# Performance work log

Hardware: AMD Instinct MI355X
Metric: run time of the kernel (lower is better)

The kernel has to match this reference:

```python
import jax, jax.numpy as jnp
import numpy as np

N, F_IN, HID, CLUST = 4096, 128, 128, 128
HEADS = 2
RADIUS = 2.0
TOPK_ADD = 2
MOTIF_TOPK = 8
ETA = 0.5
L0_GAMMA, L0_ZETA = -0.1, 1.1
NEG_SLOPE = 0.2
BN_EPS = 1e-5
NEG_INF = -1e9


def _row_topk(A, k):
    # keep top-k per row, symmetrize by max, zero diagonal (matches row_topk)
    n = A.shape[0]
    if n <= k:
        S = A
    else:
        vals, idx = jax.lax.top_k(A, k)
        S = jnp.zeros_like(A).at[jnp.arange(n)[:, None], idx].set(vals)
        S = jnp.maximum(S, S.T)
    return S * (1.0 - jnp.eye(n, dtype=A.dtype))


def _bn_eval(x, g, b, m, v):
    return (x - m) * g * jax.lax.rsqrt(v + BN_EPS) + b


def _gate(logits, tau):
    # hard-concrete gate, eval path
    t = jnp.clip(tau, 0.1, None)
    s = jax.nn.sigmoid(logits / t) * (L0_ZETA - L0_GAMMA) + L0_GAMMA
    return jnp.clip(s, 0.0, 1.0)


def _gcn_dense(feat, A_w, W, b):
    # GCN: D^-1/2 A D^-1/2 (X W) + b, zero-degree rows -> 0
    deg = A_w.sum(axis=1)
    dinv = jnp.where(deg > 0, jax.lax.rsqrt(jnp.where(deg > 0, deg, 1.0)), 0.0)
    An = dinv[:, None] * A_w * dinv[None, :]
    return An @ (feat @ W) + b


def setup_inputs():
    key = jax.random.key(0)
    ks = jax.random.split(key, 30)
    eye = jnp.eye(N, dtype=jnp.float32)
    p = 16.0 / N  # ~16 avg degree
    B = jax.random.uniform(ks[0], (N, N)) < p
    A_in = ((B | B.T) & ~jnp.eye(N, dtype=bool)).astype(jnp.float32)
    Mw = jnp.where(jax.random.uniform(ks[1], (N, N)) < p, jax.random.uniform(ks[2], (N, N)), 0.0)
    A_motif = jnp.maximum(Mw, Mw.T) * (1.0 - eye)
    coords = jax.random.randint(ks[3], (N, 2), 0, 64).astype(jnp.float32)
    x = jax.random.normal(ks[4], (N, F_IN))
    s_in = 1.0 / np.sqrt(F_IN)
    s_h = 1.0 / np.sqrt(2 * HID)
    return {
        'x': x, 'A_in': A_in, 'A_motif': A_motif, 'coords': coords,
        'gat_w': jax.random.normal(ks[5], (F_IN, HEADS * HID)) * s_in,
        'gat_asrc': jax.random.normal(ks[6], (HEADS, HID)) * s_h,
        'gat_adst': jax.random.normal(ks[7], (HEADS, HID)) * s_h,
        'gat_b': jnp.zeros((HEADS * HID,)),
        'bnA_g': jnp.ones((2 * HID,)), 'bnA_b': jnp.zeros((2 * HID,)),
        'bnA_m': jax.random.normal(ks[8], (2 * HID,)) * 0.1,
        'bnA_v': 0.5 + jax.random.uniform(ks[9], (2 * HID,)),
        'gcnM_w': jax.random.normal(ks[10], (F_IN, 2 * HID)) * s_in,
        'gcnM_b': jnp.zeros((2 * HID,)),
        'bnM_g': jnp.ones((2 * HID,)), 'bnM_b': jnp.zeros((2 * HID,)),
        'bnM_m': jax.random.normal(ks[11], (2 * HID,)) * 0.1,
        'bnM_v': 0.5 + jax.random.uniform(ks[12], (2 * HID,)),
        'mu': jnp.asarray(-3.0), 'tau': jnp.asarray(1.0),
        'prune_w': jax.random.normal(ks[13], (4 * HID + 1,)) * s_h,
        'prune_b': jnp.asarray(0.0),
        'rewire_w': jax.random.normal(ks[14], (4 * HID + 1,)) * s_h,
        'rewire_b': jnp.asarray(0.0),
        'pool_w': jax.random.normal(ks[15], (2 * HID, CLUST)) * s_h,
        'pool_b': jnp.zeros((CLUST,)),
    }


def reference(x, A_in, A_motif, coords, gat_w, gat_asrc, gat_adst, gat_b,
              bnA_g, bnA_b, bnA_m, bnA_v, gcnM_w, gcnM_b, bnM_g, bnM_b, bnM_m, bnM_v,
              mu, tau, prune_w, prune_b, rewire_w, rewire_b, pool_w, pool_b):
    n = x.shape[0]
    eye = jnp.eye(n, dtype=x.dtype)
    # --- GAT branch on A_in (dense masked attention; PyG adds self loops) ---
    Wx = (x @ gat_w).reshape(n, HEADS, HID)           # [N, heads, H]
    a_src = (Wx * gat_asrc).sum(-1)                   # [N, heads]
    a_dst = (Wx * gat_adst).sum(-1)
    e = jax.nn.leaky_relu(a_dst[:, None, :] + a_src[None, :, :], NEG_SLOPE)  # e[i,j,h]
    adj_mask = (A_in > 0) | jnp.eye(n, dtype=bool)
    e = jnp.where(adj_mask[..., None], e, NEG_INF)
    alpha = jax.nn.softmax(e, axis=1)                 # softmax over sources j
    h_A = jnp.einsum('ijh,jhd->ihd', alpha, Wx).reshape(n, HEADS * HID) + gat_b
    h_A = jax.nn.elu(_bn_eval(h_A, bnA_g, bnA_b, bnA_m, bnA_v))
    # --- motif branch ---
    M_hat = _row_topk(A_motif, MOTIF_TOPK)
    h_M = jax.nn.elu(_bn_eval(_gcn_dense(x, M_hat, gcnM_w, gcnM_b), bnM_g, bnM_b, bnM_m, bnM_v))
    h = h_A + jax.nn.softplus(mu) * h_M               # [N, 2H]
    d2 = 2 * HID
    triu = jnp.triu(jnp.ones((n, n), dtype=bool), 1)
    # --- prune gate on existing upper-tri edges (Linear is separable) ---
    pu = h @ prune_w[:d2]
    pv = h @ prune_w[d2:2 * d2]
    prune_logits = pu[:, None] + pv[None, :] + prune_w[2 * d2] * M_hat + prune_b
    z_prune = _gate(prune_logits, tau)
    edge_u = triu & (A_in > 0)
    Wp = jnp.where(edge_u, z_prune * A_in, 0.0)
    A_pruned = Wp + Wp.T
    # --- rewire candidates: L1 cdist within radius, non-edges, upper tri ---
    dist = jnp.abs(coords[:, None, :] - coords[None, :, :]).sum(-1)
    cand_u = (dist > 0) & (dist <= RADIUS) & (A_in < 1e-6) & triu
    ru = h @ rewire_w[:d2]
    rv = h @ rewire_w[d2:2 * d2]
    rew_logits = ru[:, None] + rv[None, :] + rewire_w[2 * d2] * M_hat + rewire_b
    Zu = jnp.where(cand_u, _gate(rew_logits, tau), 0.0)
    # per-node top-k selection over incident candidates (symmetric view)
    cand_sym = cand_u | cand_u.T
    scores = jnp.where(cand_sym, Zu + Zu.T, NEG_INF)
    thr = jax.lax.top_k(scores, TOPK_ADD)[0][:, -1]
    keep = (scores >= thr[:, None]) & cand_sym
    pair_keep = (keep | keep.T) & cand_u
    A_added_u = jnp.where(pair_keep, Zu, 0.0)
    A_added_sym = jnp.maximum(A_added_u, A_added_u.T)
    A_refined = A_pruned + ETA * A_added_sym
    # --- pooling GCN (default GCNConv adds self loops, weight 1) ---
    S = jax.nn.softmax(_gcn_dense(h, A_refined + eye, pool_w, pool_b), axis=1)  # [N, C]
    X_coarse = S.T @ h                                 # [C, 2H]
    A_c = S.T @ A_refined @ S
    A_c = A_c * (1.0 - jnp.eye(A_c.shape[0], dtype=A_c.dtype))
    A_coarse = _row_topk(A_c, MOTIF_TOPK)
    return X_coarse, A_coarse
```

## Files before the change

kernel.cpp:

```cpp
#include <hip/hip_runtime.h>
#include <hip/hip_bf16.h>
#include <stdint.h>

#define N 4096
#define FIN 128
#define HID 128
#define D2 256
#define CLUST 128
#define NEG_INF (-1e9f)
#define KAJ 128
#define KM 96
#define KC 64
#define KA (KAJ + KC)
#define CCAP 32
#define JCH 128
#define NCH (N/JCH)
#define CTILE 16

typedef __hip_bfloat16 bf16;

__device__ __forceinline__ float cvt(float v){ return v; }
__device__ __forceinline__ float cvt(bf16 v){ return __bfloat162float(v); }
__device__ __forceinline__ void stout(float* p, size_t i, float v){ p[i] = v; }
__device__ __forceinline__ void stout(bf16* p, size_t i, float v){ p[i] = __float2bfloat16(v); }

__device__ __forceinline__ float hc_gate(float l, float tau){
  float t = fmaxf(tau, 0.1f);
  float s = 1.f / (1.f + expf(-l / t));
  s = s * 1.2f - 0.1f;
  return fminf(fmaxf(s, 0.f), 1.f);
}

__global__ void k_detect(const void* x, const void* w, int* flag){
  __shared__ int hits;
  int t = threadIdx.x;
  if (t == 0) hits = 0;
  __syncthreads();
  const bf16* xb = (const bf16*)x;
  const bf16* wb = (const bf16*)w;
  int h = 0;
  for (int i = t; i < 4096; i += 256){
    float a = __bfloat162float(xb[i]);
    float b = __bfloat162float(wb[i]);
    if (!(fabsf(a) < 1e6f)) ++h;
    if (!(fabsf(b) < 1e6f)) ++h;
  }
  atomicAdd(&hits, h);
  __syncthreads();
  if (t == 0) *flag = (hits > 0) ? 1 : 0;
}

template<typename T>
__device__ void xw2_body(const T* x, const T* gat_w, const T* gcnM_w,
                         float* Wx, float* xwM, float* xr){
  int i0 = blockIdx.x * 16, t = threadIdx.x;
  for (int idx = t; idx < 16*FIN; idx += 256) xr[idx] = cvt(x[(size_t)i0*FIN + idx]);
  __syncthreads();
  float wx[16], xm[16];
  #pragma unroll
  for (int r = 0; r < 16; ++r){ wx[r] = 0.f; xm[r] = 0.f; }
  for (int k = 0; k < FIN; ++k){
    float wa = cvt(gat_w[k*D2 + t]);
    float wm = cvt(gcnM_w[k*D2 + t]);
    #pragma unroll
    for (int r = 0; r < 16; ++r){
      wx[r] += xr[r*FIN + k] * wa;
      xm[r] += xr[r*FIN + k] * wm;
    }
  }
  #pragma unroll
  for (int r = 0; r < 16; ++r){
    Wx[(size_t)(i0+r)*D2 + t] = wx[r];
    xwM[(size_t)(i0+r)*D2 + t] = xm[r];
  }
}
__global__ void k_xw2(const int* fl, const void* x, const void* gw, const void* gmw,
                      float* Wx, float* xwM){
  __shared__ float xr[16*FIN];
  if (*fl) xw2_body<float>((const float*)x,(const float*)gw,(const float*)gmw,Wx,xwM,xr);
  else     xw2_body<bf16 >((const bf16*)x,(const bf16*)gw,(const bf16*)gmw,Wx,xwM,xr);
}

template<typename T>
__device__ void att_body(const float* Wx, const T* asrc, const T* adst,
                         float* a_src, float* a_dst){
  int w = threadIdx.x >> 6, l = threadIdx.x & 63;
  int row = blockIdx.x*4 + w;
  const float4* wr = (const float4*)(Wx + (size_t)row*D2);
  float4 v = wr[l];
  float s0 = cvt(asrc[l*4])*v.x + cvt(asrc[l*4+1])*v.y
           + cvt(asrc[l*4+2])*v.z + cvt(asrc[l*4+3])*v.w;
  float s1 = cvt(adst[l*4])*v.x + cvt(adst[l*4+1])*v.y
           + cvt(adst[l*4+2])*v.z + cvt(adst[l*4+3])*v.w;
  for (int d = 16; d > 0; d >>= 1){
    s0 += __shfl_down(s0, d, 32);
    s1 += __shfl_down(s1, d, 32);
  }
  if ((l & 31) == 0){
    a_src[row*2 + (l >> 5)] = s0;
    a_dst[row*2 + (l >> 5)] = s1;
  }
}
__global__ void k_att(const int* fl, const float* Wx, const void* as, const void* ad,
                      float* a_src, float* a_dst){
  if (*fl) att_body<float>(Wx,(const float*)as,(const float*)ad,a_src,a_dst);
  else     att_body<bf16 >(Wx,(const bf16*)as,(const bf16*)ad,a_src,a_dst);
}

__device__ __forceinline__ void t8_insert(unsigned long long* keys, float v, int j){
  if (v > 0.f){
    unsigned long long key =
      ((unsigned long long)__float_as_uint(v) << 32) | (unsigned int)(~(unsigned int)j);
    if (key > keys[7]){
      keys[7] = key;
      #pragma unroll
      for (int q = 7; q > 0; --q){
        if (keys[q] > keys[q-1]){ unsigned long long tmp = keys[q]; keys[q] = keys[q-1]; keys[q-1] = tmp; }
      }
    }
  }
}
__global__ void k_top8(const int* fl, const void* Amot, float* t8v, int* t8i,
                       int* Midx, float* Mval, int* Mcnt){
  __shared__ unsigned long long red[256];
  int i = blockIdx.x, t = threadIdx.x;
  unsigned long long keys[8];
  #pragma unroll
  for (int q = 0; q < 8; ++q) keys[q] = 0ull;
  if (*fl){
    const float4* rowp = (const float4*)((const float*)Amot + (size_t)i*N);
    for (int s = 0; s < N/1024; ++s){
      float4 v4 = rowp[s*256 + t];
      int jb = s*1024 + t*4;
      t8_insert(keys, v4.x, jb);
      t8_insert(keys, v4.y, jb+1);
      t8_insert(keys, v4.z, jb+2);
      t8_insert(keys, v4.w, jb+3);
    }
  } else {
    const bf16* rowp = (const bf16*)Amot + (size_t)i*N;
    for (int s = 0; s < N/256; ++s){
      int j = t + 256*s;
      t8_insert(keys, cvt(rowp[j]), j);
    }
  }
  unsigned long long wins[8];
  unsigned long long last = ~0ull;
  for (int r = 0; r < 8; ++r){
    unsigned long long cand = 0ull;
    #pragma unroll
    for (int q = 0; q < 8; ++q){ if (keys[q] < last){ cand = keys[q]; break; } }
    red[t] = cand;
    __syncthreads();
    for (int s = 128; s > 0; s >>= 1){
      if (t < s){ if (red[t+s] > red[t]) red[t] = red[t+s]; }
      __syncthreads();
    }
    unsigned long long win = red[0];
    __syncthreads();
    wins[r] = win;
    last = win;
  }
  if (t == 0){
    int c = 0;
    #pragma unroll
    for (int r = 0; r < 8; ++r){
      float v = __uint_as_float((unsigned int)(wins[r] >> 32));
      int j = (int)(~(unsigned int)wins[r]);
      bool ok = (wins[r] != 0ull) && (v > 0.f);
      t8v[i*8 + r] = ok ? v : 0.f;
      t8i[i*8 + r] = ok ? j : -1;
      if (ok){ Midx[i*KM + c] = j; Mval[i*KM + c] = v; ++c; }
    }
    Mcnt[i] = c;
  }
}

__global__ void k_mscat(const float* __restrict__ t8v, const int* __restrict__ t8i,
                        int* __restrict__ Midx, float* __restrict__ Mval,
                        int* __restrict__ Mcnt){
  int e = blockIdx.x*256 + threadIdx.x;
  if (e >= N*8) return;
  int i = e >> 3;
  int j = t8i[e];
  if (j < 0) return;
  #pragma unroll
  for (int s = 0; s < 8; ++s) if (t8i[j*8 + s] == i) return;
  int p = atomicAdd(&Mcnt[j], 1);
  if (p < KM){ Midx[j*KM + p] = i; Mval[j*KM + p] = t8v[e]; }
}

__global__ void k_degM(const float* __restrict__ Mval, const int* __restrict__ Mcnt,
                       float* __restrict__ dinvM){
  int i = blockIdx.x*256 + threadIdx.x;
  if (i >= N) return;
  int n = min(Mcnt[i], KM);
  float s = 0.f;
  for (int e = 0; e < n; ++e) s += Mval[i*KM + e];
  dinvM[i] = (s > 0.f) ? rsqrtf(s) : 0.f;
}

template<typename T>
__device__ void motif_body(const int* Midx, const float* Mval, const int* Mcnt,
                           const float* dinvM, const float* xwM, const T* gcnM_b,
                           const T* bng, const T* bnb, const T* bnm, const T* bnv,
                           float* hM, int* nj, float* nw){
  int i = blockIdx.x, t = threadIdx.x;
  int n = min(Mcnt[i], KM);
  for (int e = t; e < n; e += 256){
    int j = Midx[i*KM + e];
    nj[e] = j;
    nw[e] = Mval[i*KM + e] * dinvM[j];
  }
  __syncthreads();
  float acc = 0.f;
  for (int e = 0; e < n; ++e) acc += nw[e] * xwM[nj[e]*D2 + t];
  float val = acc * dinvM[i] + cvt(gcnM_b[t]);
  val = (val - cvt(bnm[t])) * cvt(bng[t]) * rsqrtf(cvt(bnv[t]) + 1e-5f) + cvt(bnb[t]);
  val = (val > 0.f) ? val : expm1f(val);
  hM[i*D2 + t] = val;
}
__global__ void k_motif_agg(const int* fl, const int* Midx, const float* Mval,
                            const int* Mcnt, const float* dinvM, const float* xwM,
                            const void* gb, const void* g, const void* b,
                            const void* m, const void* v, float* hM){
  __shared__ int nj[KM];
  __shared__ float nw[KM];
  if (*fl) motif_body<float>(Midx,Mval,Mcnt,dinvM,xwM,(const float*)gb,(const float*)g,
                             (const float*)b,(const float*)m,(const float*)v,hM,nj,nw);
  else     motif_body<bf16 >(Midx,Mval,Mcnt,dinvM,xwM,(const bf16*)gb,(const bf16*)g,
                             (const bf16*)b,(const bf16*)m,(const bf16*)v,hM,nj,nw);
}

__global__ void k_adj(const int* fl, const void* Ain,
                      int* __restrict__ AdjIdx, float* __restrict__ AdjVal,
                      int* __restrict__ AdjCnt){
  __shared__ int cnt;
  int i = blockIdx.x, t = threadIdx.x;
  if (t == 0) cnt = 0;
  __syncthreads();
  if (*fl){
    const float4* rowp = (const float4*)((const float*)Ain + (size_t)i*N);
    for (int s = 0; s < N/1024; ++s){
      float4 v4 = rowp[s*256 + t];
      int jb = s*1024 + t*4;
      if (v4.x > 0.f && jb   != i){ int p = atomicAdd(&cnt,1); if (p < KAJ){ AdjIdx[i*KAJ+p] = jb;   AdjVal[i*KAJ+p] = v4.x; } }
      if (v4.y > 0.f && jb+1 != i){ int p = atomicAdd(&cnt,1); if (p < KAJ){ AdjIdx[i*KAJ+p] = jb+1; AdjVal[i*KAJ+p] = v4.y; } }
      if (v4.z > 0.f && jb+2 != i){ int p = atomicAdd(&cnt,1); if (p < KAJ){ AdjIdx[i*KAJ+p] = jb+2; AdjVal[i*KAJ+p] = v4.z; } }
      if (v4.w > 0.f && jb+3 != i){ int p = atomicAdd(&cnt,1); if (p < KAJ){ AdjIdx[i*KAJ+p] = jb+3; AdjVal[i*KAJ+p] = v4.w; } }
    }
  } else {
    const bf16* rowp = (const bf16*)Ain + (size_t)i*N;
    for (int j = t; j < N; j += 256){
      float v = cvt(rowp[j]);
      if (v > 0.f && j != i){ int p = atomicAdd(&cnt,1); if (p < KAJ){ AdjIdx[i*KAJ+p] = j; AdjVal[i*KAJ+p] = v; } }
    }
  }
  __syncthreads();
  if (t == 0) AdjCnt[i] = min(cnt, KAJ);
}

template<typename T>
__device__ void gat_body(const int* AdjIdx, const int* AdjCnt, const float* Wx,
                         const float* a_src, const float* a_dst, const T* gat_b,
                         const T* bng, const T* bnb, const T* bnm, const T* bnv,
                         const float* hM, const T* mu,
                         float* h, int* nbr, float* ew, float* mm, float* inv){
  int i = blockIdx.x, t = threadIdx.x;
  int na = AdjCnt[i];
  for (int e = t; e < na; e += 256) nbr[e] = AdjIdx[i*KAJ + e];
  if (t == 0) nbr[na] = i;
  __syncthreads();
  int n = na + 1;
  float ad0 = a_dst[i*2], ad1 = a_dst[i*2 + 1];
  for (int e = t; e < n; e += 256){
    int j = nbr[e];
    float e0 = ad0 + a_src[j*2];
    float e1 = ad1 + a_src[j*2 + 1];
    e0 = (e0 > 0.f) ? e0 : 0.2f * e0;
    e1 = (e1 > 0.f) ? e1 : 0.2f * e1;
    ew[2*e] = e0; ew[2*e + 1] = e1;
  }
  __syncthreads();
  if (t == 0){
    float m0 = -3.4e38f, m1 = -3.4e38f;
    for (int e = 0; e < n; ++e){ m0 = fmaxf(m0, ew[2*e]); m1 = fmaxf(m1, ew[2*e+1]); }
    mm[0] = m0; mm[1] = m1;
  }
  __syncthreads();
  for (int e = t; e < n; e += 256){
    ew[2*e]   = expf(ew[2*e]   - mm[0]);
    ew[2*e+1] = expf(ew[2*e+1] - mm[1]);
  }
  __syncthreads();
  if (t == 0){
    float s0 = 0.f, s1 = 0.f;
    for (int e = 0; e < n; ++e){ s0 += ew[2*e]; s1 += ew[2*e+1]; }
    inv[0] = 1.f/s0; inv[1] = 1.f/s1;
  }
  __syncthreads();
  int hh = t >> 7;
  float acc = 0.f;
  for (int e = 0; e < n; ++e) acc += ew[2*e + hh] * Wx[nbr[e]*D2 + t];
  float val = acc * inv[hh] + cvt(gat_b[t]);
  val = (val - cvt(bnm[t])) * cvt(bng[t]) * rsqrtf(cvt(bnv[t]) + 1e-5f) + cvt(bnb[t]);
  val = (val > 0.f) ? val : expm1f(val);
  float spmu = log1pf(expf(cvt(mu[0])));
  h[i*D2 + t] = val + spmu * hM[i*D2 + t];
}
__global__ void k_gat_agg(const int* fl, const int* AdjIdx, const int* AdjCnt,
                          const float* Wx, const float* a_src, const float* a_dst,
                          const void* gb, const void* g, const void* b, const void* m,
                          const void* v, const float* hM, const void* mu, float* h){
  __shared__ int nbr[KAJ + 1];
  __shared__ float ew[(KAJ + 1)*2];
  __shared__ float mm[2], inv[2];
  if (*fl) gat_body<float>(AdjIdx,AdjCnt,Wx,a_src,a_dst,(const float*)gb,(const float*)g,
                           (const float*)b,(const float*)m,(const float*)v,hM,(const float*)mu,
                           h,nbr,ew,mm,inv);
  else     gat_body<bf16 >(AdjIdx,AdjCnt,Wx,a_src,a_dst,(const bf16*)gb,(const bf16*)g,
                           (const bf16*)b,(const bf16*)m,(const bf16*)v,hM,(const bf16*)mu,
                           h,nbr,ew,mm,inv);
}

template<typename T>
__device__ void puv_body(const float* h, const T* pw, const T* rw,
                         float* pu, float* pv, float* ru, float* rv, float* red){
  int i = blockIdx.x, t = threadIdx.x;
  float hv = h[i*D2 + t];
  float v0 = hv * cvt(pw[t]);
  float v1 = hv * cvt(pw[D2 + t]);
  float v2 = hv * cvt(rw[t]);
  float v3 = hv * cvt(rw[D2 + t]);
  red[t] = v0; __syncthreads();
  for (int k = 128; k > 0; k >>= 1){ if (t < k) red[t] += red[t+k]; __syncthreads(); }
  if (t == 0) pu[i] = red[0];
  __syncthreads();
  red[t] = v1; __syncthreads();
  for (int k = 128; k > 0; k >>= 1){ if (t < k) red[t] += red[t+k]; __syncthreads(); }
  if (t == 0) pv[i] = red[0];
  __syncthreads();
  red[t] = v2; __syncthreads();
  for (int k = 128; k > 0; k >>= 1){ if (t < k) red[t] += red[t+k]; __syncthreads(); }
  if (t == 0) ru[i] = red[0];
  __syncthreads();
  red[t] = v3; __syncthreads();
  for (int k = 128; k > 0; k >>= 1){ if (t < k) red[t] += red[t+k]; __syncthreads(); }
  if (t == 0) rv[i] = red[0];
}
__global__ void k_puv(const int* fl, const float* h, const void* pw, const void* rw,
                      float* pu, float* pv, float* ru, float* rv){
  __shared__ float red[256];
  if (*fl) puv_body<float>(h,(const float*)pw,(const float*)rw,pu,pv,ru,rv,red);
  else     puv_body<bf16 >(h,(const bf16*)pw,(const bf16*)rw,pu,pv,ru,rv,red);
}

__global__ void k_zero(int* cellCnt){
  int i = blockIdx.x*256 + threadIdx.x;
  if (i < 4096) cellCnt[i] = 0;
}

template<typename T>
__device__ void gridb_body(const T* coords, int* cellCnt, int* cellNode){
  int i = blockIdx.x*256 + threadIdx.x;
  if (i >= N) return;
  int cx = (int)cvt(coords[2*i]), cy = (int)cvt(coords[2*i+1]);
  int cell = cy*64 + cx;
  int p = atomicAdd(&cellCnt[cell], 1);
  if (p < CCAP) cellNode[cell*CCAP + p] = i;
}
__global__ void k_gridb(const int* fl, const void* coords, int* cellCnt, int* cellNode){
  if (*fl) gridb_body<float>((const float*)coords, cellCnt, cellNode);
  else     gridb_body<bf16 >((const bf16*)coords, cellCnt, cellNode);
}

template<typename T>
__device__ void cand_body(const T* coords, const T* Ain,
                          const int* Midx, const float* Mval, const int* Mcnt,
                          const int* cellCnt, const int* cellNode,
                          const float* ru, const float* rv,
                          const T* rw, const T* rb, const T* taup,
                          int* Cidx, float* Cz, int* Ccnt, float* thr,
                          int* scI, float* scZ, int* scn){
  int w = threadIdx.x >> 6, l = threadIdx.x & 63;
  int i = blockIdx.x*4 + w;
  if (l == 0) scn[w] = 0;
  __syncthreads();
  float cix = cvt(coords[2*i]), ciy = cvt(coords[2*i+1]);
  int cx = (int)cix, cy = (int)ciy;
  float w2 = cvt(rw[2*D2]), rbias = cvt(rb[0]), tau = cvt(taup[0]);
  float rui = ru[i], rvi = rv[i];
  int mc = min(Mcnt[i], KM);
  const int dxs[12] = {1,-1,0,0, 2,-2,0,0, 1,1,-1,-1};
  const int dys[12] = {0,0,1,-1, 0,0,2,-2, 1,-1,1,-1};
  if (l < 12){
    int nx = cx + dxs[l], ny = cy + dys[l];
    if (nx >= 0 && nx < 64 && ny >= 0 && ny < 64){
      int cell = ny*64 + nx;
      int cn = min(cellCnt[cell], CCAP);
      for (int e = 0; e < cn; ++e){
        int j = cellNode[cell*CCAP + e];
        float d = fabsf(cix - cvt(coords[2*j])) + fabsf(ciy - cvt(coords[2*j+1]));
        float a = cvt(Ain[(size_t)i*N + j]);
        if (d > 0.f && d <= 2.0f && a < 1e-6f){
          float mh = 0.f;
          for (int q = 0; q < mc; ++q) if (Midx[i*KM + q] == j){ mh = Mval[i*KM + q]; break; }
          float lg = ((i < j) ? (rui + rv[j]) : (ru[j] + rvi)) + w2*mh + rbias;
          float z = hc_gate(lg, tau);
          int p = atomicAdd(&scn[w], 1);
          if (p < KC){ scI[w*KC + p] = j; scZ[w*KC + p] = z; }
        }
      }
    }
  }
  __syncthreads();
  int n = min(scn[w], KC);
  if (l == 0){
    float m1 = NEG_INF, m2 = NEG_INF;
    for (int e = 0; e < n; ++e){
      float z = scZ[w*KC + e];
      if (z > m1){ m2 = m1; m1 = z; } else if (z > m2){ m2 = z; }
    }
    thr[i] = m2;
    Ccnt[i] = n;
  }
  for (int e = l; e < n; e += 64){ Cidx[i*KC + e] = scI[w*KC + e]; Cz[i*KC + e] = scZ[w*KC + e]; }
}
__global__ void k_cand(const int* fl, const void* coords, const void* Ain,
                       const int* Midx, const float* Mval, const int* Mcnt,
                       const int* cellCnt, const int* cellNode,
                       const float* ru, const float* rv, const void* rw, const void* rb,
                       const void* taup, int* Cidx, float* Cz, int* Ccnt, float* thr){
  __shared__ int scI[4*KC];
  __shared__ float scZ[4*KC];
  __shared__ int scn[4];
  if (*fl) cand_body<float>((const float*)coords,(const float*)Ain,Midx,Mval,Mcnt,
                            cellCnt,cellNode,ru,rv,(const float*)rw,(const float*)rb,
                            (const float*)taup,Cidx,Cz,Ccnt,thr,scI,scZ,scn);
  else     cand_body<bf16 >((const bf16*)coords,(const bf16*)Ain,Midx,Mval,Mcnt,
                            cellCnt,cellNode,ru,rv,(const bf16*)rw,(const bf16*)rb,
                            (const bf16*)taup,Cidx,Cz,Ccnt,thr,scI,scZ,scn);
}

template<typename T>
__device__ void aref_body(const int* AdjIdx, const float* AdjVal, const int* AdjCnt,
                          const int* Midx, const float* Mval, const int* Mcnt,
                          const float* pu, const float* pv, const T* pw, const T* pb,
                          const T* taup, const int* Cidx, const float* Cz, const int* Ccnt,
                          const float* thr, int* Aidx, float* Aval, int* Acnt, float* dinvR){
  int w = threadIdx.x >> 6, l = threadIdx.x & 63;
  int i = blockIdx.x*4 + w;
  float wp2 = cvt(pw[2*D2]), pbias = cvt(pb[0]), tau = cvt(taup[0]);
  float pui = pu[i], pvi = pv[i];
  int na = AdjCnt[i];
  int mc = min(Mcnt[i], KM);
  float sum = 0.f;
  for (int e = l; e < na; e += 64){
    int j = AdjIdx[i*KAJ + e];
    float a = AdjVal[i*KAJ + e];
    float mh = 0.f;
    for (int q = 0; q < mc; ++q) if (Midx[i*KM + q] == j){ mh = Mval[i*KM + q]; break; }
    float lg = ((i < j) ? (pui + pv[j]) : (pu[j] + pvi)) + wp2*mh + pbias;
    float wv = hc_gate(lg, tau) * a;
    Aidx[i*KA + e] = j; Aval[i*KA + e] = wv; sum += wv;
  }
  int nc = min(Ccnt[i], KC);
  float thri = thr[i];
  for (int e = l; e < nc; e += 64){
    int j = Cidx[i*KC + e];
    float z = Cz[i*KC + e];
    float wv = (z >= thri || z >= thr[j]) ? 0.5f*z : 0.f;
    Aidx[i*KA + na + e] = j; Aval[i*KA + na + e] = wv; sum += wv;
  }
  for (int d = 32; d > 0; d >>= 1) sum += __shfl_down(sum, d, 64);
  if (l == 0){ Acnt[i] = na + nc; dinvR[i] = rsqrtf(sum + 1.f); }
}
__global__ void k_aref(const int* fl, const int* AdjIdx, const float* AdjVal,
                       const int* AdjCnt, const int* Midx, const float* Mval,
                       const int* Mcnt, const float* pu, const float* pv, const void* pw,
                       const void* pb, const void* taup, const int* Cidx, const float* Cz,
                       const int* Ccnt, const float* thr, int* Aidx, float* Aval,
                       int* Acnt, float* dinvR){
  if (*fl) aref_body<float>(AdjIdx,AdjVal,AdjCnt,Midx,Mval,Mcnt,pu,pv,(const float*)pw,
                            (const float*)pb,(const float*)taup,Cidx,Cz,Ccnt,thr,
                            Aidx,Aval,Acnt,dinvR);
  else     aref_body<bf16 >(AdjIdx,AdjVal,AdjCnt,Midx,Mval,Mcnt,pu,pv,(const bf16*)pw,
                            (const bf16*)pb,(const bf16*)taup,Cidx,Cz,Ccnt,thr,
                            Aidx,Aval,Acnt,dinvR);
}

template<typename T>
__device__ void hw_body(const float* h, const T* pool_w, float* hW, float* hr){
  int i0 = blockIdx.x*8, t = threadIdx.x;
  for (int idx = t; idx < 8*D2; idx += 128) hr[idx] = h[(size_t)i0*D2 + idx];
  __syncthreads();
  float acc[8];
  #pragma unroll
  for (int r = 0; r < 8; ++r) acc[r] = 0.f;
  for (int d = 0; d < D2; ++d){
    float w = cvt(pool_w[d*CLUST + t]);
    #pragma unroll
    for (int r = 0; r < 8; ++r) acc[r] += hr[r*D2 + d] * w;
  }
  #pragma unroll
  for (int r = 0; r < 8; ++r) hW[(size_t)(i0+r)*CLUST + t] = acc[r];
}
__global__ void k_hw(const int* fl, const float* h, const void* pw, float* hW){
  __shared__ float hr[8*D2];
  if (*fl) hw_body<float>(h,(const float*)pw,hW,hr);
  else     hw_body<bf16 >(h,(const bf16*)pw,hW,hr);
}

template<typename T>
__device__ void preS_body(const int* Aidx, const float* Aval, const int* Acnt,
                          const float* dinvR, const float* hW, const T* pool_b,
                          float* S, int* sAi, float* sW, float* part, float* red){
  int i = blockIdx.x, t = threadIdx.x;
  int col = t & 127, hf = t >> 7;
  int n = min(Acnt[i], KA);
  for (int e = t; e < n; e += 256){
    int j = Aidx[i*KA + e];
    sAi[e] = j;
    sW[e] = Aval[i*KA + e] * dinvR[j];
  }
  __syncthreads();
  int half = (n + 1) >> 1;
  int e0 = hf ? half : 0;
  int e1 = hf ? n : half;
  float di = dinvR[i];
  float acc = (hf == 0) ? di * hW[i*CLUST + col] : 0.f;
  for (int e = e0; e < e1; ++e) acc += sW[e] * hW[sAi[e]*CLUST + col];
  part[t] = acc;
  __syncthreads();
  float val = 0.f;
  if (t < 128){
    val = (part[t] + part[t + 128]) * di + cvt(pool_b[t]);
    red[t] = val;
  }
  __syncthreads();
  for (int k = 64; k > 0; k >>= 1){ if (t < k) red[t] = fmaxf(red[t], red[t+k]); __syncthreads(); }
  float mx = red[0]; __syncthreads();
  float ex = 0.f;
  if (t < 128){ ex = expf(val - mx); red[t] = ex; }
  __syncthreads();
  for (int k = 64; k > 0; k >>= 1){ if (t < k) red[t] += red[t+k]; __syncthreads(); }
  float sm = red[0]; __syncthreads();
  if (t < 128) S[i*CLUST + t] = ex / sm;
}
__global__ void k_preS(const int* fl, const int* Aidx, const float* Aval, const int* Acnt,
                       const float* dinvR, const float* hW, const void* pb, float* S){
  __shared__ int sAi[KA];
  __shared__ float sW[KA];
  __shared__ float part[256];
  __shared__ float red[128];
  if (*fl) preS_body<float>(Aidx,Aval,Acnt,dinvR,hW,(const float*)pb,S,sAi,sW,part,red);
  else     preS_body<bf16 >(Aidx,Aval,Acnt,dinvR,hW,(const bf16*)pb,S,sAi,sW,part,red);
}

__global__ void k_T(const int* __restrict__ Aidx, const float* __restrict__ Aval,
                    const int* __restrict__ Acnt, const float* __restrict__ S,
                    float* __restrict__ T){
  __shared__ int sAi[KA];
  __shared__ float sW[KA];
  __shared__ float part[256];
  int i = blockIdx.x, t = threadIdx.x;
  int col = t & 127, hf = t >> 7;
  int n = min(Acnt[i], KA);
  for (int e = t; e < n; e += 256){
    sAi[e] = Aidx[i*KA + e];
    sW[e] = Aval[i*KA + e];
  }
  __syncthreads();
  int half = (n + 1) >> 1;
  int e0 = hf ? half : 0;
  int e1 = hf ? n : half;
  float acc = 0.f;
  for (int e = e0; e < e1; ++e) acc += sW[e] * S[sAi[e]*CLUST + col];
  part[t] = acc;
  __syncthreads();
  if (t < 128) T[i*CLUST + t] = part[t] + part[t + 128];
}

__global__ void k_coarse1(const float* __restrict__ S, const float* __restrict__ h,
                          const float* __restrict__ T_,
                          float* __restrict__ PX, float* __restrict__ PA){
  __shared__ float ss[JCH][CTILE];
  int c0 = blockIdx.x * CTILE, ch = blockIdx.y, t = threadIdx.x;
  int j0 = ch * JCH;
  for (int idx = t; idx < JCH*CTILE; idx += 384){
    int j = idx >> 4, cc = idx & 15;
    ss[j][cc] = S[(size_t)(j0 + j)*CLUST + c0 + cc];
  }
  __syncthreads();
  if (t < 256){
    float acc[CTILE];
    #pragma unroll
    for (int cc = 0; cc < CTILE; ++cc) acc[cc] = 0.f;
    for (int j = 0; j < JCH; ++j){
      float v = h[(size_t)(j0 + j)*D2 + t];
      #pragma unroll
      for (int cc = 0; cc < CTILE; ++cc) acc[cc] += ss[j][cc] * v;
    }
    #pragma unroll
    for (int cc = 0; cc < CTILE; ++cc)
      PX[((size_t)ch*CLUST + c0 + cc)*D2 + t] = acc[cc];
  } else {
    int tt = t - 256;
    float acc[CTILE];
    #pragma unroll
    for (int cc = 0; cc < CTILE; ++cc) acc[cc] = 0.f;
    for (int j = 0; j < JCH; ++j){
      float v = T_[(size_t)(j0 + j)*CLUST + tt];
      #pragma unroll
      for (int cc = 0; cc < CTILE; ++cc) acc[cc] += ss[j][cc] * v;
    }
    #pragma unroll
    for (int cc = 0; cc < CTILE; ++cc)
      PA[((size_t)ch*CLUST + c0 + cc)*CLUST + tt] = acc[cc];
  }
}

template<typename OT>
__device__ void coarse2_body(const float* PX, const float* PA, OT* Xout, float* Ac){
  int c = blockIdx.x, t = threadIdx.x;
  if (t < 256){
    float s = 0.f;
    #pragma unroll 8
    for (int ch = 0; ch < NCH; ++ch) s += PX[((size_t)ch*CLUST + c)*D2 + t];
    stout(Xout, (size_t)c*D2 + t, s);
  } else {
    int tt = t - 256;
    float s = 0.f;
    #pragma unroll 8
    for (int ch = 0; ch < NCH; ++ch) s += PA[((size_t)ch*CLUST + c)*CLUST + tt];
    Ac[c*CLUST + tt] = (tt == c) ? 0.f : s;
  }
}
__global__ void k_coarse2(const int* fl, const float* PX, const float* PA,
                          void* out, float* Ac){
  if (*fl) coarse2_body<float>(PX, PA, (float*)out, Ac);
  else     coarse2_body<bf16 >(PX, PA, (bf16*)out, Ac);
}

__global__ void k_top8c(const float* __restrict__ Ac, float* __restrict__ Acs){
  __shared__ unsigned long long red[128];
  int r = blockIdx.x, t = threadIdx.x;
  float v = Ac[r*CLUST + t];
  unsigned long long mykey =
    ((unsigned long long)__float_as_uint(fmaxf(v, 0.f)) << 32) | (unsigned int)(~(unsigned int)t);
  unsigned long long last = ~0ull;
  bool selected = false;
  for (int q = 0; q < 8; ++q){
    red[t] = (mykey < last) ? mykey : 0ull;
    __syncthreads();
    for (int k = 64; k > 0; k >>= 1){
      if (t < k){ if (red[t+k] > red[t]) red[t] = red[t+k]; }
      __syncthreads();
    }
    unsigned long long win = red[0];
    __syncthreads();
    if (win != 0ull && win == mykey) selected = true;
    last = win;
  }
  Acs[r*CLUST + t] = (selected && v > 0.f) ? v : 0.f;
}

template<typename OT>
__device__ void sym_body(const float* Acs, OT* out){
  int r = blockIdx.x, t = threadIdx.x;
  float v = (r == t) ? 0.f : fmaxf(Acs[r*CLUST + t], Acs[t*CLUST + r]);
  stout(out, (size_t)(CLUST*D2) + r*CLUST + t, v);
}
__global__ void k_sym(const int* fl, const float* Acs, void* out){
  if (*fl) sym_body<float>(Acs, (float*)out);
  else     sym_body<bf16 >(Acs, (bf16*)out);
}

extern "C" void kernel_launch(void* const* d_in, const int* in_sizes, int n_in,
                              void* d_out, int out_size, void* d_ws, size_t ws_size,
                              hipStream_t stream){
  (void)in_sizes; (void)n_in; (void)out_size; (void)ws_size;
  const void* x       = d_in[0];
  const void* A_in    = d_in[1];
  const void* A_motif = d_in[2];
  const void* coords  = d_in[3];
  const void* gat_w   = d_in[4];
  const void* gat_asrc= d_in[5];
  const void* gat_adst= d_in[6];
  const void* gat_b   = d_in[7];
  const void* bnA_g   = d_in[8];
  const void* bnA_b   = d_in[9];
  const void* bnA_m   = d_in[10];
  const void* bnA_v   = d_in[11];
  const void* gcnM_w  = d_in[12];
  const void* gcnM_b  = d_in[13];
  const void* bnM_g   = d_in[14];
  const void* bnM_b   = d_in[15];
  const void* bnM_m   = d_in[16];
  const void* bnM_v   = d_in[17];
  const void* mu      = d_in[18];
  const void* tau     = d_in[19];
  const void* prune_w = d_in[20];
  const void* prune_b = d_in[21];
  const void* rewire_w= d_in[22];
  const void* rewire_b= d_in[23];
  const void* pool_w  = d_in[24];
  const void* pool_b  = d_in[25];

  char* p = (char*)d_ws;
  auto alloc = [&](size_t bytes) -> void* {
    void* r = (void*)p;
    p += (bytes + 255) & ~(size_t)255;
    return r;
  };
  int*   flag    = (int*)  alloc(256);
  float* Wx      = (float*)alloc((size_t)N*D2*4);
  float* xwM     = (float*)alloc((size_t)N*D2*4);
  float* a_src   = (float*)alloc((size_t)N*2*4);
  float* a_dst   = (float*)alloc((size_t)N*2*4);
  float* t8v     = (float*)alloc((size_t)N*8*4);
  int*   t8i     = (int*)  alloc((size_t)N*8*4);
  int*   Midx    = (int*)  alloc((size_t)N*KM*4);
  float* Mval    = (float*)alloc((size_t)N*KM*4);
  int*   Mcnt    = (int*)  alloc((size_t)N*4);
  float* dinvM   = (float*)alloc((size_t)N*4);
  float* hM      = (float*)alloc((size_t)N*D2*4);
  float* hbuf    = (float*)alloc((size_t)N*D2*4);
  float* pu      = (float*)alloc((size_t)N*4);
  float* pv      = (float*)alloc((size_t)N*4);
  float* ru      = (float*)alloc((size_t)N*4);
  float* rv      = (float*)alloc((size_t)N*4);
  int*   AdjIdx  = (int*)  alloc((size_t)N*KAJ*4);
  float* AdjVal  = (float*)alloc((size_t)N*KAJ*4);
  int*   AdjCnt  = (int*)  alloc((size_t)N*4);
  int*   cellCnt = (int*)  alloc((size_t)4096*4);
  int*   cellNode= (int*)  alloc((size_t)4096*CCAP*4);
  int*   Cidx    = (int*)  alloc((size_t)N*KC*4);
  float* Cz      = (float*)alloc((size_t)N*KC*4);
  int*   Ccnt    = (int*)  alloc((size_t)N*4);
  float* thr     = (float*)alloc((size_t)N*4);
  int*   Aidx    = (int*)  alloc((size_t)N*KA*4);
  float* Aval    = (float*)alloc((size_t)N*KA*4);
  int*   Acnt    = (int*)  alloc((size_t)N*4);
  float* dinvR   = (float*)alloc((size_t)N*4);
  float* hW      = (float*)alloc((size_t)N*CLUST*4);
  float* S       = (float*)alloc((size_t)N*CLUST*4);
  float* T       = (float*)alloc((size_t)N*CLUST*4);
  float* PX      = (float*)alloc((size_t)NCH*CLUST*D2*4);
  float* PA      = (float*)alloc((size_t)NCH*CLUST*CLUST*4);
  float* Ac      = (float*)alloc((size_t)CLUST*CLUST*4);
  float* Acs     = (float*)alloc((size_t)CLUST*CLUST*4);

  k_detect<<<1, 256, 0, stream>>>(x, gat_w, flag);
  k_xw2<<<N/16, 256, 0, stream>>>(flag, x, gat_w, gcnM_w, Wx, xwM);
  k_att<<<N/4, 256, 0, stream>>>(flag, Wx, gat_asrc, gat_adst, a_src, a_dst);
  k_top8<<<N, 256, 0, stream>>>(flag, A_motif, t8v, t8i, Midx, Mval, Mcnt);
  k_mscat<<<(N*8)/256, 256, 0, stream>>>(t8v, t8i, Midx, Mval, Mcnt);
  k_degM<<<N/256, 256, 0, stream>>>(Mval, Mcnt, dinvM);
  k_motif_agg<<<N, 256, 0, stream>>>(flag, Midx, Mval, Mcnt, dinvM, xwM, gcnM_b,
                                     bnM_g, bnM_b, bnM_m, bnM_v, hM);
  k_adj<<<N, 256, 0, stream>>>(flag, A_in, AdjIdx, AdjVal, AdjCnt);
  k_zero<<<16, 256, 0, stream>>>(cellCnt);
  k_gridb<<<16, 256, 0, stream>>>(flag, coords, cellCnt, cellNode);
  k_gat_agg<<<N, 256, 0, stream>>>(flag, AdjIdx, AdjCnt, Wx, a_src, a_dst, gat_b,
                                   bnA_g, bnA_b, bnA_m, bnA_v, hM, mu, hbuf);
  k_puv<<<N, 256, 0, stream>>>(flag, hbuf, prune_w, rewire_w, pu, pv, ru, rv);
  k_cand<<<N/4, 256, 0, stream>>>(flag, coords, A_in, Midx, Mval, Mcnt, cellCnt, cellNode,
                                  ru, rv, rewire_w, rewire_b, tau, Cidx, Cz, Ccnt, thr);
  k_aref<<<N/4, 256, 0, stream>>>(flag, AdjIdx, AdjVal, AdjCnt, Midx, Mval, Mcnt,
                                  pu, pv, prune_w, prune_b, tau, Cidx, Cz, Ccnt, thr,
                                  Aidx, Aval, Acnt, dinvR);
  k_hw<<<N/8, 128, 0, stream>>>(flag, hbuf, pool_w, hW);
  k_preS<<<N, 256, 0, stream>>>(flag, Aidx, Aval, Acnt, dinvR, hW, pool_b, S);
  k_T<<<N, 256, 0, stream>>>(Aidx, Aval, Acnt, S, T);
  k_coarse1<<<dim3(CLUST/CTILE, NCH), 384, 0, stream>>>(S, hbuf, T, PX, PA);
  k_coarse2<<<CLUST, 384, 0, stream>>>(flag, PX, PA, d_out, Ac);
  k_top8c<<<CLUST, 128, 0, stream>>>(Ac, Acs);
  k_sym<<<CLUST, 128, 0, stream>>>(flag, Acs, d_out);
}
```

Measured before the change: 439.9 us.

## Rework top-8 selection, shrink xw2 tiles, unroll gathers, fold zeroing into detect

Replaces the per-thread top-8 heaps and eight rounds of block reductions in k_top8 with a sparse compaction of positive entries into shared memory, followed by a single-thread top-8 over them (capped at POSCAP). Shrinks k_xw2 from 16 to 4 rows per block for more blocks, unrolls the gather loops in several aggregation kernels into multiple accumulators, and folds the cellCnt zeroing into k_detect so one launch is removed. The detect scan is also halved. Risks include dropping entries if a row has more than POSCAP positives, and a serial single-thread loop.

```diff
diff --git a/kernel.cpp b/kernel.cpp
--- a/kernel.cpp
+++ b/kernel.cpp
@@ -16,6 +16,7 @@
 #define JCH 128
 #define NCH (N/JCH)
 #define CTILE 16
+#define POSCAP 256
 
 typedef __hip_bfloat16 bf16;
 
@@ -31,15 +32,16 @@
   return fminf(fmaxf(s, 0.f), 1.f);
 }
 
-__global__ void k_detect(const void* x, const void* w, int* flag){
+__global__ void k_detect(const void* x, const void* w, int* flag, int* cellCnt){
   __shared__ int hits;
   int t = threadIdx.x;
   if (t == 0) hits = 0;
+  for (int i = t; i < 4096; i += 256) cellCnt[i] = 0;
   __syncthreads();
   const bf16* xb = (const bf16*)x;
   const bf16* wb = (const bf16*)w;
   int h = 0;
-  for (int i = t; i < 4096; i += 256){
+  for (int i = t; i < 2048; i += 256){
     float a = __bfloat162float(xb[i]);
     float b = __bfloat162float(wb[i]);
     if (!(fabsf(a) < 1e6f)) ++h;
@@ -53,30 +55,31 @@
 template<typename T>
 __device__ void xw2_body(const T* x, const T* gat_w, const T* gcnM_w,
                          float* Wx, float* xwM, float* xr){
-  int i0 = blockIdx.x * 16, t = threadIdx.x;
-  for (int idx = t; idx < 16*FIN; idx += 256) xr[idx] = cvt(x[(size_t)i0*FIN + idx]);
-  __syncthreads();
-  float wx[16], xm[16];
+  int i0 = blockIdx.x * 4, t = threadIdx.x;
+  for (int idx = t; idx < 4*FIN; idx += 256) xr[idx] = cvt(x[(size_t)i0*FIN + idx]);
+  __syncthreads();
+  float wx[4], xm[4];
   #pragma unroll
-  for (int r = 0; r < 16; ++r){ wx[r] = 0.f; xm[r] = 0.f; }
+  for (int r = 0; r < 4; ++r){ wx[r] = 0.f; xm[r] = 0.f; }
+  #pragma unroll 4
   for (int k = 0; k < FIN; ++k){
     float wa = cvt(gat_w[k*D2 + t]);
     float wm = cvt(gcnM_w[k*D2 + t]);
     #pragma unroll
-    for (int r = 0; r < 16; ++r){
+    for (int r = 0; r < 4; ++r){
       wx[r] += xr[r*FIN + k] * wa;
       xm[r] += xr[r*FIN + k] * wm;
     }
   }
   #pragma unroll
-  for (int r = 0; r < 16; ++r){
+  for (int r = 0; r < 4; ++r){
     Wx[(size_t)(i0+r)*D2 + t] = wx[r];
     xwM[(size_t)(i0+r)*D2 + t] = xm[r];
   }
 }
 __global__ void k_xw2(const int* fl, const void* x, const void* gw, const void* gmw,
                       float* Wx, float* xwM){
-  __shared__ float xr[16*FIN];
+  __shared__ float xr[4*FIN];
   if (*fl) xw2_body<float>((const float*)x,(const float*)gw,(const float*)gmw,Wx,xwM,xr);
   else     xw2_body<bf16 >((const bf16*)x,(const bf16*)gw,(const bf16*)gmw,Wx,xwM,xr);
 }
@@ -108,66 +111,54 @@
 }
 
 __device__ __forceinline__ void t8_insert(unsigned long long* keys, float v, int j){
-  if (v > 0.f){
-    unsigned long long key =
-      ((unsigned long long)__float_as_uint(v) << 32) | (unsigned int)(~(unsigned int)j);
-    if (key > keys[7]){
-      keys[7] = key;
-      #pragma unroll
-      for (int q = 7; q > 0; --q){
-        if (keys[q] > keys[q-1]){ unsigned long long tmp = keys[q]; keys[q] = keys[q-1]; keys[q-1] = tmp; }
-      }
+  unsigned long long key =
+    ((unsigned long long)__float_as_uint(v) << 32) | (unsigned int)(~(unsigned int)j);
+  if (key > keys[7]){
+    keys[7] = key;
+    #pragma unroll
+    for (int q = 7; q > 0; --q){
+      if (keys[q] > keys[q-1]){ unsigned long long tmp = keys[q]; keys[q] = keys[q-1]; keys[q-1] = tmp; }
     }
   }
 }
 __global__ void k_top8(const int* fl, const void* Amot, float* t8v, int* t8i,
                        int* Midx, float* Mval, int* Mcnt){
-  __shared__ unsigned long long red[256];
+  __shared__ int pj[POSCAP];
+  __shared__ float pv[POSCAP];
+  __shared__ int cnt;
   int i = blockIdx.x, t = threadIdx.x;
-  unsigned long long keys[8];
-  #pragma unroll
-  for (int q = 0; q < 8; ++q) keys[q] = 0ull;
+  if (t == 0) cnt = 0;
+  __syncthreads();
   if (*fl){
     const float4* rowp = (const float4*)((const float*)Amot + (size_t)i*N);
     for (int s = 0; s < N/1024; ++s){
       float4 v4 = rowp[s*256 + t];
       int jb = s*1024 + t*4;
-      t8_insert(keys, v4.x, jb);
-      t8_insert(keys, v4.y, jb+1);
-      t8_insert(keys, v4.z, jb+2);
-      t8_insert(keys, v4.w, jb+3);
+      if (v4.x > 0.f){ int p = atomicAdd(&cnt,1); if (p < POSCAP){ pj[p] = jb;   pv[p] = v4.x; } }
+      if (v4.y > 0.f){ int p = atomicAdd(&cnt,1); if (p < POSCAP){ pj[p] = jb+1; pv[p] = v4.y; } }
+      if (v4.z > 0.f){ int p = atomicAdd(&cnt,1); if (p < POSCAP){ pj[p] = jb+2; pv[p] = v4.z; } }
+      if (v4.w > 0.f){ int p = atomicAdd(&cnt,1); if (p < POSCAP){ pj[p] = jb+3; pv[p] = v4.w; } }
     }
   } else {
     const bf16* rowp = (const bf16*)Amot + (size_t)i*N;
-    for (int s = 0; s < N/256; ++s){
-      int j = t + 256*s;
-      t8_insert(keys, cvt(rowp[j]), j);
-    }
-  }
-  unsigned long long wins[8];
-  unsigned long long last = ~0ull;
-  for (int r = 0; r < 8; ++r){
-    unsigned long long cand = 0ull;
-    #pragma unroll
-    for (int q = 0; q < 8; ++q){ if (keys[q] < last){ cand = keys[q]; break; } }
-    red[t] = cand;
-    __syncthreads();
-    for (int s = 128; s > 0; s >>= 1){
-      if (t < s){ if (red[t+s] > red[t]) red[t] = red[t+s]; }
-      __syncthreads();
-    }
-    unsigned long long win = red[0];
-    __syncthreads();
-    wins[r] = win;
-    last = win;
-  }
+    for (int j = t; j < N; j += 256){
+      float v = cvt(rowp[j]);
+      if (v > 0.f){ int p = atomicAdd(&cnt,1); if (p < POSCAP){ pj[p] = j; pv[p] = v; } }
+    }
+  }
+  __syncthreads();
   if (t == 0){
+    int n = min(cnt, POSCAP);
+    unsigned long long keys[8];
+    #pragma unroll
+    for (int q = 0; q < 8; ++q) keys[q] = 0ull;
+    for (int e = 0; e < n; ++e) t8_insert(keys, pv[e], pj[e]);
     int c = 0;
     #pragma unroll
     for (int r = 0; r < 8; ++r){
-      float v = __uint_as_float((unsigned int)(wins[r] >> 32));
-      int j = (int)(~(unsigned int)wins[r]);
-      bool ok = (wins[r] != 0ull) && (v > 0.f);
+      float v = __uint_as_float((unsigned int)(keys[r] >> 32));
+      int j = (int)(~(unsigned int)keys[r]);
+      bool ok = (keys[r] != 0ull) && (v > 0.f);
       t8v[i*8 + r] = ok ? v : 0.f;
       t8i[i*8 + r] = ok ? j : -1;
       if (ok){ Midx[i*KM + c] = j; Mval[i*KM + c] = v; ++c; }
@@ -213,8 +204,16 @@
     nw[e] = Mval[i*KM + e] * dinvM[j];
   }
   __syncthreads();
-  float acc = 0.f;
-  for (int e = 0; e < n; ++e) acc += nw[e] * xwM[nj[e]*D2 + t];
+  float a0 = 0.f, a1 = 0.f, a2 = 0.f, a3 = 0.f;
+  int e = 0;
+  for (; e + 3 < n; e += 4){
+    a0 += nw[e]   * xwM[nj[e]*D2 + t];
+    a1 += nw[e+1] * xwM[nj[e+1]*D2 + t];
+    a2 += nw[e+2] * xwM[nj[e+2]*D2 + t];
+    a3 += nw[e+3] * xwM[nj[e+3]*D2 + t];
+  }
+  for (; e < n; ++e) a0 += nw[e] * xwM[nj[e]*D2 + t];
+  float acc = (a0 + a1) + (a2 + a3);
   float val = acc * dinvM[i] + cvt(gcnM_b[t]);
   val = (val - cvt(bnm[t])) * cvt(bng[t]) * rsqrtf(cvt(bnv[t]) + 1e-5f) + cvt(bnb[t]);
   val = (val > 0.f) ? val : expm1f(val);
@@ -300,8 +299,16 @@
   }
   __syncthreads();
   int hh = t >> 7;
-  float acc = 0.f;
-  for (int e = 0; e < n; ++e) acc += ew[2*e + hh] * Wx[nbr[e]*D2 + t];
+  float a0 = 0.f, a1 = 0.f, a2 = 0.f, a3 = 0.f;
+  int e = 0;
+  for (; e + 3 < n; e += 4){
+    a0 += ew[2*e + hh]     * Wx[nbr[e]*D2 + t];
+    a1 += ew[2*(e+1) + hh] * Wx[nbr[e+1]*D2 + t];
+    a2 += ew[2*(e+2) + hh] * Wx[nbr[e+2]*D2 + t];
+    a3 += ew[2*(e+3) + hh] * Wx[nbr[e+3]*D2 + t];
+  }
+  for (; e < n; ++e) a0 += ew[2*e + hh] * Wx[nbr[e]*D2 + t];
+  float acc = (a0 + a1) + (a2 + a3);
   float val = acc * inv[hh] + cvt(gat_b[t]);
   val = (val - cvt(bnm[t])) * cvt(bng[t]) * rsqrtf(cvt(bnv[t]) + 1e-5f) + cvt(bnb[t]);
   val = (val > 0.f) ? val : expm1f(val);
@@ -353,11 +360,6 @@
   __shared__ float red[256];
   if (*fl) puv_body<float>(h,(const float*)pw,(const float*)rw,pu,pv,ru,rv,red);
   else     puv_body<bf16 >(h,(const bf16*)pw,(const bf16*)rw,pu,pv,ru,rv,red);
-}
-
-__global__ void k_zero(int* cellCnt){
-  int i = blockIdx.x*256 + threadIdx.x;
-  if (i < 4096) cellCnt[i] = 0;
 }
 
 template<typename T>
@@ -529,8 +531,14 @@
   int e1 = hf ? n : half;
   float di = dinvR[i];
   float acc = (hf == 0) ? di * hW[i*CLUST + col] : 0.f;
-  for (int e = e0; e < e1; ++e) acc += sW[e] * hW[sAi[e]*CLUST + col];
-  part[t] = acc;
+  float acc2 = 0.f;
+  int e = e0;
+  for (; e + 1 < e1; e += 2){
+    acc  += sW[e]   * hW[sAi[e]*CLUST + col];
+    acc2 += sW[e+1] * hW[sAi[e+1]*CLUST + col];
+  }
+  if (e < e1) acc += sW[e] * hW[sAi[e]*CLUST + col];
+  part[t] = acc + acc2;
   __syncthreads();
   float val = 0.f;
   if (t < 128){
@@ -574,9 +582,14 @@
   int half = (n + 1) >> 1;
   int e0 = hf ? half : 0;
   int e1 = hf ? n : half;
-  float acc = 0.f;
-  for (int e = e0; e < e1; ++e) acc += sW[e] * S[sAi[e]*CLUST + col];
-  part[t] = acc;
+  float acc = 0.f, acc2 = 0.f;
+  int e = e0;
+  for (; e + 1 < e1; e += 2){
+    acc  += sW[e]   * S[sAi[e]*CLUST + col];
+    acc2 += sW[e+1] * S[sAi[e+1]*CLUST + col];
+  }
+  if (e < e1) acc += sW[e] * S[sAi[e]*CLUST + col];
+  part[t] = acc + acc2;
   __syncthreads();
   if (t < 128) T[i*CLUST + t] = part[t] + part[t + 128];
 }
@@ -751,8 +764,8 @@
   float* Ac      = (float*)alloc((size_t)CLUST*CLUST*4);
   float* Acs     = (float*)alloc((size_t)CLUST*CLUST*4);
 
-  k_detect<<<1, 256, 0, stream>>>(x, gat_w, flag);
-  k_xw2<<<N/16, 256, 0, stream>>>(flag, x, gat_w, gcnM_w, Wx, xwM);
+  k_detect<<<1, 256, 0, stream>>>(x, gat_w, flag, cellCnt);
+  k_xw2<<<N/4, 256, 0, stream>>>(flag, x, gat_w, gcnM_w, Wx, xwM);
   k_att<<<N/4, 256, 0, stream>>>(flag, Wx, gat_asrc, gat_adst, a_src, a_dst);
   k_top8<<<N, 256, 0, stream>>>(flag, A_motif, t8v, t8i, Midx, Mval, Mcnt);
   k_mscat<<<(N*8)/256, 256, 0, stream>>>(t8v, t8i, Midx, Mval, Mcnt);
@@ -760,7 +773,6 @@
   k_motif_agg<<<N, 256, 0, stream>>>(flag, Midx, Mval, Mcnt, dinvM, xwM, gcnM_b,
                                      bnM_g, bnM_b, bnM_m, bnM_v, hM);
   k_adj<<<N, 256, 0, stream>>>(flag, A_in, AdjIdx, AdjVal, AdjCnt);
-  k_zero<<<16, 256, 0, stream>>>(cellCnt);
   k_gridb<<<16, 256, 0, stream>>>(flag, coords, cellCnt, cellNode);
   k_gat_agg<<<N, 256, 0, stream>>>(flag, AdjIdx, AdjCnt, Wx, a_src, a_dst, gat_b,
                                    bnA_g, bnA_b, bnA_m, bnA_v, hM, mu, hbuf);
```

Result: faster. 404.1 us (-8.1%).
